# Performance work log

Measured on AMD Instinct MI355X. Metric: run time of the kernel, lower is better.

## Reference

```python
import jax, jax.numpy as jnp
import numpy as np

N_HEAD = 16
ROPE_BASE = 10000.0


def rope_cos_sin(T, head_dim, dtype):
    inv_freq = 1.0 / (ROPE_BASE ** (jnp.arange(0, head_dim, 2, dtype=jnp.float32) / head_dim))
    t = jnp.arange(T, dtype=jnp.float32)
    freqs = jnp.einsum('i,j->ij', t, inv_freq)          # [T, head_dim/2]
    emb = jnp.concatenate([freqs, freqs], axis=-1)       # [T, head_dim]
    return jnp.cos(emb).astype(dtype), jnp.sin(emb).astype(dtype)


def rotate_half(x):
    h = x.shape[-1] // 2
    return jnp.concatenate([-x[..., h:], x[..., :h]], axis=-1)


def setup_inputs() -> dict:
    key = jax.random.key(0)
    ks = jax.random.split(key, 5)
    B, T, C = 2, 1024, 2048
    s = 0.02
    return {
        'x': jax.random.normal(ks[0], (B, T, C), dtype=jnp.float32),
        'Wq': jax.random.normal(ks[1], (C, C), dtype=jnp.float32) * s,
        'Wk': jax.random.normal(ks[2], (C, C), dtype=jnp.float32) * s,
        'Wv': jax.random.normal(ks[3], (C, C), dtype=jnp.float32) * s,
        'Wo': jax.random.normal(ks[4], (C, C), dtype=jnp.float32) * s,
    }


def reference(x, Wq, Wk, Wv, Wo):
    B, T, C = x.shape
    H = N_HEAD
    D = C // H
    # torch Linear: y = x @ W.T  (W is [out, in])
    q = jnp.einsum('btc,oc->bto', x, Wq).reshape(B, T, H, D).transpose(0, 2, 1, 3)
    k = jnp.einsum('btc,oc->bto', x, Wk).reshape(B, T, H, D).transpose(0, 2, 1, 3)
    v = jnp.einsum('btc,oc->bto', x, Wv).reshape(B, T, H, D).transpose(0, 2, 1, 3)
    cos, sin = rope_cos_sin(T, D, x.dtype)               # [T, D]
    cos = cos[None, None]                                 # [1,1,T,D]
    sin = sin[None, None]
    q = q * cos + rotate_half(q) * sin
    k = k * cos + rotate_half(k) * sin
    scale = 1.0 / jnp.sqrt(jnp.asarray(D, dtype=x.dtype))
    att = jnp.einsum('bhqd,bhkd->bhqk', q, k) * scale    # [B,H,T,T]
    causal = jnp.tril(jnp.ones((T, T), dtype=bool))
    att = jnp.where(causal[None, None], att, jnp.finfo(x.dtype).min)
    att = jax.nn.softmax(att, axis=-1)
    y = jnp.einsum('bhqk,bhkd->bhqd', att, v)            # [B,H,T,D]
    y = y.transpose(0, 2, 1, 3).reshape(B, T, C)
    return jnp.einsum('btc,oc->bto', y, Wo)
```

## Files before the change

kernel.cpp:

```cpp
#include <hip/hip_runtime.h>
#include <stdint.h>

typedef unsigned short u16;
typedef __bf16 bf16x8 __attribute__((ext_vector_type(8)));
typedef float  f32x4  __attribute__((ext_vector_type(4)));

#define B_  2
#define T_  1024
#define C_  2048
#define H_  16
#define D_  128
#define NTENS 4194304

__device__ __forceinline__ u16 f2bf(float f) {
    union { float f; uint32_t u; } v; v.f = f;
    uint32_t r = (v.u + 0x7FFFu + ((v.u >> 16) & 1u)) >> 16;
    return (u16)r;
}
__device__ __forceinline__ float bf2f(u16 h) {
    union { uint32_t u; float f; } v; v.u = ((uint32_t)h) << 16;
    return v.f;
}

__global__ __launch_bounds__(256) void k_convert(
    const float* __restrict__ x, const float* __restrict__ wq,
    const float* __restrict__ wk, const float* __restrict__ wv,
    const float* __restrict__ wo, u16* __restrict__ dst)
{
    int z = blockIdx.z;
    const float* src = (z == 0) ? x : (z == 1) ? wq : (z == 2) ? wk : (z == 3) ? wv : wo;
    u16* d = dst + (size_t)z * NTENS;
    size_t i = ((size_t)blockIdx.x * 256 + threadIdx.x) * 4;
    float4 v = *(const float4*)(src + i);
    ushort4 o;
    o.x = f2bf(v.x); o.y = f2bf(v.y); o.z = f2bf(v.z); o.w = f2bf(v.w);
    *(ushort4*)(d + i) = o;
}

__global__ void k_rope_table(float* __restrict__ ct, float* __restrict__ st)
{
    int t = blockIdx.x, d = threadIdx.x;
    float inv = expf(-(float)d * (9.210340371976184f / 64.0f));
    float th = (float)t * inv;
    float s, c;
    sincosf(th, &s, &c);
    ct[t * 64 + d] = c;
    st[t * 64 + d] = s;
}

template<int MTILE, int EPI>
__device__ __forceinline__ void gemm_tile_nt(
    const u16* __restrict__ A, int lda,
    const u16* __restrict__ Bp, int ldb,
    void* __restrict__ Cp, int ldc,
    int m0, int n0, int K,
    u16* SMEM, const float* __restrict__ ct, const float* __restrict__ st, int z)
{
    constexpr int MF  = MTILE / 16;
    constexpr int ACH = MTILE / 32;
    u16* As = SMEM;
    u16* Bs = SMEM + MTILE * 64;

    const int tid  = threadIdx.x;
    const int wave = tid >> 6;
    const int lane = tid & 63;
    const int frow = lane & 15;
    const int quad = lane >> 4;

    const int lrow8  = lane >> 3;
    const int slot   = lane & 7;
    const int gchunk = slot ^ lrow8;

    f32x4 acc[MF][2] = {};

    size_t aoff[ACH], boff[4];
#pragma unroll
    for (int i = 0; i < ACH; ++i) {
        int c = (i << 2) + wave;
        int r = (c << 3) + lrow8;
        aoff[i] = (size_t)(m0 + r) * lda + (gchunk << 3);
    }
#pragma unroll
    for (int i = 0; i < 4; ++i) {
        int r = (i << 5) + (wave << 3) + lrow8;
        boff[i] = (size_t)(n0 + r) * ldb + (gchunk << 3);
    }

    for (int kt = 0; kt < K; kt += 64) {
#pragma unroll
        for (int i = 0; i < ACH; ++i) {
            int c = (i << 2) + wave;
            __builtin_amdgcn_global_load_lds(
                (const __attribute__((address_space(1))) void*)(A + aoff[i] + kt),
                (__attribute__((address_space(3))) void*)(As + (c << 9)), 16, 0, 0);
        }
#pragma unroll
        for (int i = 0; i < 4; ++i) {
            int c = (i << 2) + wave;
            __builtin_amdgcn_global_load_lds(
                (const __attribute__((address_space(1))) void*)(Bp + boff[i] + kt),
                (__attribute__((address_space(3))) void*)(Bs + (c << 9)), 16, 0, 0);
        }
        __syncthreads();

#pragma unroll
        for (int ks = 0; ks < 2; ++ks) {
            int lk = (ks << 2) + quad;
            bf16x8 af[MF], bfv[2];
#pragma unroll
            for (int i = 0; i < MF; ++i) {
                int ar = (i << 4) + frow;
                af[i] = *(const bf16x8*)&As[ar * 64 + ((lk ^ (frow & 7)) << 3)];
            }
#pragma unroll
            for (int j = 0; j < 2; ++j) {
                int br = (wave << 4) + (j << 6) + frow;
                bfv[j] = *(const bf16x8*)&Bs[br * 64 + ((lk ^ (frow & 7)) << 3)];
            }
#pragma unroll
            for (int i = 0; i < MF; ++i)
#pragma unroll
                for (int j = 0; j < 2; ++j)
                    acc[i][j] = __builtin_amdgcn_mfma_f32_16x16x32_bf16(
                        af[i], bfv[j], acc[i][j], 0, 0, 0);
        }
        __syncthreads();
    }

    if constexpr (EPI == 2) {
        if (z < 2) {
            const int d = (wave << 4) + frow;
            const float sc = (z == 0) ? 0.08838834764831845f : 1.0f;
            u16* Op = (u16*)Cp;
#pragma unroll
            for (int i = 0; i < MF; ++i)
#pragma unroll
                for (int r = 0; r < 4; ++r) {
                    int m = m0 + (i << 4) + (quad << 2) + r;
                    int t = m & 1023;
                    float c = ct[t * 64 + d], s = st[t * 64 + d];
                    float a = acc[i][0][r], bb = acc[i][1][r];
                    Op[(size_t)m * ldc + n0 + d]      = f2bf((a * c - bb * s) * sc);
                    Op[(size_t)m * ldc + n0 + d + 64] = f2bf((bb * c + a * s) * sc);
                }
            return;
        }
    }

#pragma unroll
    for (int i = 0; i < MF; ++i)
#pragma unroll
        for (int j = 0; j < 2; ++j)
#pragma unroll
            for (int r = 0; r < 4; ++r) {
                int m = m0 + (i << 4) + (quad << 2) + r;
                int n = n0 + (wave << 4) + (j << 6) + frow;
                if constexpr (EPI == 0)
                    ((float*)Cp)[(size_t)m * ldc + n] = acc[i][j][r];
                else
                    ((u16*)Cp)[(size_t)m * ldc + n] = f2bf(acc[i][j][r]);
            }
}

__global__ __launch_bounds__(256) void k_gemm_qkv(
    const u16* __restrict__ xb, const u16* __restrict__ wq,
    const u16* __restrict__ wk, const u16* __restrict__ wv,
    u16* __restrict__ q, u16* __restrict__ k, u16* __restrict__ v,
    const float* __restrict__ ct, const float* __restrict__ st)
{
    __shared__ u16 SMEM[64 * 64 + 128 * 64];
    int z = blockIdx.z;
    const u16* Bp = (z == 0) ? wq : (z == 1) ? wk : wv;
    u16* Op       = (z == 0) ? q  : (z == 1) ? k  : v;
    gemm_tile_nt<64, 2>(xb, C_, Bp, C_, Op, C_,
                        blockIdx.y * 64, blockIdx.x * 128, C_, SMEM, ct, st, z);
}

__global__ __launch_bounds__(256) void k_flash(
    const u16* __restrict__ qb, const u16* __restrict__ kb,
    const u16* __restrict__ vb, u16* __restrict__ yb)
{
    __shared__ u16 Ks[128 * 128];
    __shared__ u16 Vs[128 * 128];

    const int bx  = blockIdx.x;
    const int bh  = bx & 31, b = bh >> 4, h = bh & 15;
    const int qt  = (bx < 256) ? (15 - (bx >> 5)) : ((bx >> 5) - 8);
    const int KT  = (qt >> 1) + 1;
    const int tid = threadIdx.x, wave = tid >> 6, lane = tid & 63;
    const int frow = lane & 15, quad = lane >> 4;

    const u16* qbase = qb + (size_t)b * (T_ * C_) + h * D_;
    const u16* kbase = kb + (size_t)b * (T_ * C_) + h * D_;
    const u16* vbase = vb + (size_t)b * (T_ * C_) + h * D_;
    const int q0 = qt << 6;

    bf16x8 qf[4];
#pragma unroll
    for (int ks = 0; ks < 4; ++ks)
        qf[ks] = *(const bf16x8*)&qbase[(size_t)(q0 + (wave << 4) + frow) * C_
                                        + (ks << 5) + (quad << 3)];

    f32x4 Y[8] = {};
    float mrow[4], lrow[4];
#pragma unroll
    for (int r = 0; r < 4; ++r) { mrow[r] = -3e38f; lrow[r] = 0.f; }

    const int tok = q0 + (wave << 4) + (quad << 2);

    for (int kt = 0; kt < KT; ++kt) {
        const int k0 = kt << 7;
        {
            const int r4 = lane >> 4, s16 = lane & 15;
#pragma unroll
            for (int i = 0; i < 8; ++i) {
                int c = (i << 2) + wave;
                int row = (c << 2) + r4;
                int g = (s16 & 8) | ((s16 & 7) ^ (row & 7));
                __builtin_amdgcn_global_load_lds(
                    (const __attribute__((address_space(1))) void*)(kbase + (size_t)(k0 + row) * C_ + (g << 3)),
                    (__attribute__((address_space(3))) void*)(Ks + (c << 9)), 16, 0, 0);
            }
        }
        {
#pragma unroll
            for (int i = 0; i < 8; ++i) {
                int idx = (i << 8) + tid;
                int kr  = idx & 127;
                int n8  = (idx >> 7) << 3;
                uint4 vv = *(const uint4*)&vbase[(size_t)(k0 + kr) * C_ + n8];
                u16 tmp[8];
                *(uint4*)tmp = vv;
                int s = kr >> 3, t7 = kr & 7;
#pragma unroll
                for (int e = 0; e < 8; ++e) {
                    int d = n8 + e;
                    int swz = (s & 8) | ((s & 7) ^ (d & 7));
                    Vs[d * 128 + (swz << 3) + t7] = tmp[e];
                }
            }
        }
        __syncthreads();

        f32x4 S[8] = {};
#pragma unroll
        for (int ks = 0; ks < 4; ++ks) {
            int lk = (ks << 2) + quad;
            int sw = ((lk & 8) | ((lk & 7) ^ (frow & 7))) << 3;
#pragma unroll
            for (int jj = 0; jj < 8; ++jj) {
                bf16x8 bb = *(const bf16x8*)&Ks[((jj << 4) + frow) * 128 + sw];
                S[jj] = __builtin_amdgcn_mfma_f32_16x16x32_bf16(qf[ks], bb, S[jj], 0, 0, 0);
            }
        }

        if (kt == KT - 1) {
#pragma unroll
            for (int jj = 0; jj < 8; ++jj) {
                int colg = k0 + (jj << 4) + frow;
#pragma unroll
                for (int r = 0; r < 4; ++r)
                    if (colg > tok + r) S[jj][r] = -1e30f;
            }
        }

        float al[4];
#pragma unroll
        for (int r = 0; r < 4; ++r) {
            float tm = -3e38f;
#pragma unroll
            for (int jj = 0; jj < 8; ++jj) tm = fmaxf(tm, S[jj][r]);
#pragma unroll
            for (int off = 8; off > 0; off >>= 1) tm = fmaxf(tm, __shfl_xor(tm, off));
            float mn = fmaxf(mrow[r], tm);
            al[r] = __expf(mrow[r] - mn);
            mrow[r] = mn;
            float rs = 0.f;
#pragma unroll
            for (int jj = 0; jj < 8; ++jj) {
                float e = __expf(S[jj][r] - mn);
                S[jj][r] = e;
                rs += e;
            }
#pragma unroll
            for (int off = 8; off > 0; off >>= 1) rs += __shfl_xor(rs, off);
            lrow[r] = lrow[r] * al[r] + rs;
        }
#pragma unroll
        for (int dj = 0; dj < 8; ++dj)
#pragma unroll
            for (int r = 0; r < 4; ++r) Y[dj][r] *= al[r];

        __syncthreads();

        u16* Ps = Ks;
#pragma unroll
        for (int jj = 0; jj < 8; ++jj)
#pragma unroll
            for (int r = 0; r < 4; ++r)
                Ps[((wave << 4) + (quad << 2) + r) * 136 + (jj << 4) + frow] = f2bf(S[jj][r]);

#pragma unroll
        for (int ks = 0; ks < 4; ++ks) {
            bf16x8 pa = *(const bf16x8*)&Ps[((wave << 4) + frow) * 136 + (ks << 5) + (quad << 3)];
            int lk = (ks << 2) + quad;
            int sw = ((lk & 8) | ((lk & 7) ^ (frow & 7))) << 3;
#pragma unroll
            for (int dj = 0; dj < 8; ++dj) {
                bf16x8 vv = *(const bf16x8*)&Vs[((dj << 4) + frow) * 128 + sw];
                Y[dj] = __builtin_amdgcn_mfma_f32_16x16x32_bf16(pa, vv, Y[dj], 0, 0, 0);
            }
        }
        __syncthreads();
    }

    u16* ybase = yb + (size_t)b * (T_ * C_) + h * D_;
#pragma unroll
    for (int r = 0; r < 4; ++r) {
        float inv = 1.0f / lrow[r];
#pragma unroll
        for (int dj = 0; dj < 8; ++dj)
            ybase[(size_t)(tok + r) * C_ + (dj << 4) + frow] = f2bf(Y[dj][r] * inv);
    }
}

__global__ __launch_bounds__(256) void k_gemm_out(
    const u16* __restrict__ yb, const u16* __restrict__ wo, float* __restrict__ out)
{
    __shared__ u16 SMEM[64 * 64 + 128 * 64];
    gemm_tile_nt<64, 0>(yb, C_, wo, C_, out, C_,
                        blockIdx.y * 64, blockIdx.x * 128, C_, SMEM, nullptr, nullptr, 0);
}

extern "C" void kernel_launch(void* const* d_in, const int* in_sizes, int n_in,
                              void* d_out, int out_size, void* d_ws, size_t ws_size,
                              hipStream_t stream)
{
    (void)in_sizes; (void)n_in; (void)out_size; (void)ws_size;
    const float* x  = (const float*)d_in[0];
    const float* Wq = (const float*)d_in[1];
    const float* Wk = (const float*)d_in[2];
    const float* Wv = (const float*)d_in[3];
    const float* Wo = (const float*)d_in[4];

    u16* ws  = (u16*)d_ws;
    u16* xb  = ws;
    u16* wqb = ws + (size_t)1 * NTENS;
    u16* wkb = ws + (size_t)2 * NTENS;
    u16* wvb = ws + (size_t)3 * NTENS;
    u16* wob = ws + (size_t)4 * NTENS;
    u16* qb  = ws + (size_t)5 * NTENS;
    u16* kb  = ws + (size_t)6 * NTENS;
    u16* vb  = ws + (size_t)7 * NTENS;
    u16* yb  = ws + (size_t)8 * NTENS;
    float* ct = (float*)(ws + (size_t)9 * NTENS);
    float* st = ct + 65536;

    k_convert   <<<dim3(4096, 1, 5), 256, 0, stream>>>(x, Wq, Wk, Wv, Wo, ws);
    k_rope_table<<<dim3(1024), 64, 0, stream>>>(ct, st);
    k_gemm_qkv  <<<dim3(16, 32, 3), 256, 0, stream>>>(xb, wqb, wkb, wvb, qb, kb, vb, ct, st);
    k_flash     <<<dim3(512), 256, 0, stream>>>(qb, kb, vb, yb);
    k_gemm_out  <<<dim3(16, 32, 1), 256, 0, stream>>>(yb, wob, (float*)d_out);
}
```

Measured before the change: 262.9 us.

## Pre-transpose V into head-major layout and async-load it in flash kernel

Adds a separate kernel that transposes V into a per-head [D, T] layout, so the flash kernel can load V tiles with the same swizzled async global-to-LDS loads it already uses for K. This replaces the per-element scalar LDS scatter stores that transposed V inside every flash block's inner loop. It also folds the RoPE table computation into the convert kernel to save one launch. The trade-off is an extra kernel launch plus one more read and write of V through global memory.

```diff
diff --git a/kernel.cpp b/kernel.cpp
--- a/kernel.cpp
+++ b/kernel.cpp
@@ -25,9 +25,23 @@
 __global__ __launch_bounds__(256) void k_convert(
     const float* __restrict__ x, const float* __restrict__ wq,
     const float* __restrict__ wk, const float* __restrict__ wv,
-    const float* __restrict__ wo, u16* __restrict__ dst)
+    const float* __restrict__ wo, u16* __restrict__ dst,
+    float* __restrict__ ct, float* __restrict__ st)
 {
     int z = blockIdx.z;
+    if (z == 5) {
+        int idx = blockIdx.x * 256 + threadIdx.x;
+        if (idx < 65536) {
+            int t = idx >> 6, d = idx & 63;
+            float inv = expf(-(float)d * (9.210340371976184f / 64.0f));
+            float th = (float)t * inv;
+            float s, c;
+            sincosf(th, &s, &c);
+            ct[idx] = c;
+            st[idx] = s;
+        }
+        return;
+    }
     const float* src = (z == 0) ? x : (z == 1) ? wq : (z == 2) ? wk : (z == 3) ? wv : wo;
     u16* d = dst + (size_t)z * NTENS;
     size_t i = ((size_t)blockIdx.x * 256 + threadIdx.x) * 4;
@@ -37,15 +51,35 @@
     *(ushort4*)(d + i) = o;
 }
 
-__global__ void k_rope_table(float* __restrict__ ct, float* __restrict__ st)
-{
-    int t = blockIdx.x, d = threadIdx.x;
-    float inv = expf(-(float)d * (9.210340371976184f / 64.0f));
-    float th = (float)t * inv;
-    float s, c;
-    sincosf(th, &s, &c);
-    ct[t * 64 + d] = c;
-    st[t * 64 + d] = s;
+__global__ __launch_bounds__(256) void k_transpose_v(
+    const u16* __restrict__ vb, u16* __restrict__ vt)
+{
+    __shared__ u16 L[64 * 136];
+    int t0 = blockIdx.x << 6;
+    int bh = blockIdx.y, b = bh >> 4, h = bh & 15;
+    const u16* src = vb + (size_t)b * (T_ * C_) + h * D_;
+    u16* dst = vt + (size_t)bh * (D_ * T_);
+    int tid = threadIdx.x;
+#pragma unroll
+    for (int i = 0; i < 4; ++i) {
+        int idx = (i << 8) + tid;
+        int r = idx >> 4, s = idx & 15;
+        *(uint4*)&L[r * 136 + (s << 3)] =
+            *(const uint4*)&src[(size_t)(t0 + r) * C_ + (s << 3)];
+    }
+    __syncthreads();
+#pragma unroll
+    for (int i = 0; i < 8; ++i) {
+        int idx = (i << 8) + tid;
+        int d = idx >> 4, s = idx & 15;
+        int t = s << 2;
+        ushort4 o;
+        o.x = L[(t    ) * 136 + d];
+        o.y = L[(t + 1) * 136 + d];
+        o.z = L[(t + 2) * 136 + d];
+        o.w = L[(t + 3) * 136 + d];
+        *(ushort4*)&dst[(size_t)d * T_ + t0 + t] = o;
+    }
 }
 
 template<int MTILE, int EPI>
@@ -178,7 +212,7 @@
 
 __global__ __launch_bounds__(256) void k_flash(
     const u16* __restrict__ qb, const u16* __restrict__ kb,
-    const u16* __restrict__ vb, u16* __restrict__ yb)
+    const u16* __restrict__ vt, u16* __restrict__ yb)
 {
     __shared__ u16 Ks[128 * 128];
     __shared__ u16 Vs[128 * 128];
@@ -192,7 +226,7 @@
 
     const u16* qbase = qb + (size_t)b * (T_ * C_) + h * D_;
     const u16* kbase = kb + (size_t)b * (T_ * C_) + h * D_;
-    const u16* vbase = vb + (size_t)b * (T_ * C_) + h * D_;
+    const u16* vbase = vt + (size_t)bh * (D_ * T_);
     const int q0 = qt << 6;
 
     bf16x8 qf[4];
@@ -220,24 +254,9 @@
                 __builtin_amdgcn_global_load_lds(
                     (const __attribute__((address_space(1))) void*)(kbase + (size_t)(k0 + row) * C_ + (g << 3)),
                     (__attribute__((address_space(3))) void*)(Ks + (c << 9)), 16, 0, 0);
-            }
-        }
-        {
-#pragma unroll
-            for (int i = 0; i < 8; ++i) {
-                int idx = (i << 8) + tid;
-                int kr  = idx & 127;
-                int n8  = (idx >> 7) << 3;
-                uint4 vv = *(const uint4*)&vbase[(size_t)(k0 + kr) * C_ + n8];
-                u16 tmp[8];
-                *(uint4*)tmp = vv;
-                int s = kr >> 3, t7 = kr & 7;
-#pragma unroll
-                for (int e = 0; e < 8; ++e) {
-                    int d = n8 + e;
-                    int swz = (s & 8) | ((s & 7) ^ (d & 7));
-                    Vs[d * 128 + (swz << 3) + t7] = tmp[e];
-                }
+                __builtin_amdgcn_global_load_lds(
+                    (const __attribute__((address_space(1))) void*)(vbase + (size_t)row * T_ + k0 + (g << 3)),
+                    (__attribute__((address_space(3))) void*)(Vs + (c << 9)), 16, 0, 0);
             }
         }
         __syncthreads();
@@ -353,12 +372,13 @@
     u16* kb  = ws + (size_t)6 * NTENS;
     u16* vb  = ws + (size_t)7 * NTENS;
     u16* yb  = ws + (size_t)8 * NTENS;
-    float* ct = (float*)(ws + (size_t)9 * NTENS);
+    u16* vt  = ws + (size_t)9 * NTENS;
+    float* ct = (float*)(ws + (size_t)10 * NTENS);
     float* st = ct + 65536;
 
-    k_convert   <<<dim3(4096, 1, 5), 256, 0, stream>>>(x, Wq, Wk, Wv, Wo, ws);
-    k_rope_table<<<dim3(1024), 64, 0, stream>>>(ct, st);
-    k_gemm_qkv  <<<dim3(16, 32, 3), 256, 0, stream>>>(xb, wqb, wkb, wvb, qb, kb, vb, ct, st);
-    k_flash     <<<dim3(512), 256, 0, stream>>>(qb, kb, vb, yb);
-    k_gemm_out  <<<dim3(16, 32, 1), 256, 0, stream>>>(yb, wob, (float*)d_out);
-}
+    k_convert    <<<dim3(4096, 1, 6), 256, 0, stream>>>(x, Wq, Wk, Wv, Wo, ws, ct, st);
+    k_gemm_qkv   <<<dim3(16, 32, 3), 256, 0, stream>>>(xb, wqb, wkb, wvb, qb, kb, vb, ct, st);
+    k_transpose_v<<<dim3(16, 32), 256, 0, stream>>>(vb, vt);
+    k_flash      <<<dim3(512), 256, 0, stream>>>(qb, kb, vt, yb);
+    k_gemm_out   <<<dim3(16, 32, 1), 256, 0, stream>>>(yb, wob, (float*)d_out);
+}
```

After: 259.9 us. No clear change (-1.1%).
